# Optimization experiments

Measured on AMD Instinct MI355X. Metric: run time of the kernel, lower is better.

Reference implementation:

```python
import jax, jax.numpy as jnp
import numpy as np

B, L, D_MODEL, H = 2, 1920, 512, 8
DEPTH = D_MODEL // H
MAX_REL = 1921


def skew(t):
    """Huang et al. 2018 skew: pad, reshape, slice. t: (..., L, L)."""
    Lq, Lk = t.shape[-2], t.shape[-1]
    padded = jnp.pad(t, [(0, 0)] * (t.ndim - 1) + [(1, 0)])  # (..., Lq, Lk+1)
    s = padded.reshape(-1, Lk + 1, Lq)[:, 1:]                 # drop first row
    return s.reshape(t.shape)


def setup_inputs() -> dict:
    key = jax.random.key(0)
    ks = jax.random.split(key, 12)
    w = lambda k, shp: (jax.random.normal(k, shp, jnp.float32) * 0.02)
    inp = {
        "q": jax.random.normal(ks[0], (B, L, D_MODEL), jnp.float32),
        "k": jax.random.normal(ks[1], (B, L, D_MODEL), jnp.float32),
        "v": jax.random.normal(ks[2], (B, L, D_MODEL), jnp.float32),
        "mask": jnp.triu(jnp.ones((L, L), jnp.float32), k=1)[None, None],  # causal look-ahead
        "Wq": w(ks[3], (D_MODEL, D_MODEL)), "bq": jnp.zeros((D_MODEL,), jnp.float32),
        "Wk": w(ks[4], (D_MODEL, D_MODEL)), "bk": jnp.zeros((D_MODEL,), jnp.float32),
        "Wv": w(ks[5], (D_MODEL, D_MODEL)), "bv": jnp.zeros((D_MODEL,), jnp.float32),
        "E": w(ks[6], (MAX_REL, D_MODEL)),
        "Wo": w(ks[7], (D_MODEL, D_MODEL)), "bo": jnp.zeros((D_MODEL,), jnp.float32),
    }
    return inp


def reference(q, k, v, mask, Wq, bq, Wk, bk, Wv, bv, E, Wo, bo):
    Lk = k.shape[-2]
    qp = q @ Wq + bq
    kp = k @ Wk + bk
    vp = v @ Wv + bv
    # required relative embeddings (max_len >= seq_len branch): rightmost Lk rows
    e = E[MAX_REL - Lk:]                                   # (Lk, d_model)
    # split heads
    qh = qp.reshape(B, -1, H, DEPTH).transpose(0, 2, 1, 3)  # (B,H,Lq,depth)
    kh = kp.reshape(B, Lk, H, DEPTH).transpose(0, 2, 1, 3)
    vh = vp.reshape(B, Lk, H, DEPTH).transpose(0, 2, 1, 3)
    eh = e.reshape(Lk, H, DEPTH).transpose(1, 0, 2)         # (H,Lk,depth)
    QKt = jnp.einsum('bhqd,bhkd->bhqk', qh, kh)
    Srel = skew(jnp.einsum('bhqd,hkd->bhqk', qh, eh))
    logits = (QKt + Srel) / jnp.sqrt(jnp.float32(DEPTH))
    logits = logits + mask * (-1e9)
    attn = jax.nn.softmax(logits, axis=-1)                  # (B,H,Lq,Lk)
    out = jnp.einsum('bhqk,bhkd->bhqd', attn, vh)
    out = out.transpose(0, 2, 1, 3).reshape(B, -1, D_MODEL)
    out = out @ Wo + bo
    return out, attn
```

## Files before the change

kernel.cpp:

```cpp
#include <hip/hip_runtime.h>

typedef unsigned short u16;
typedef short s16x8 __attribute__((ext_vector_type(8)));
typedef float f32x4 __attribute__((ext_vector_type(4)));

#define MFMA_BF16(a, b, c) __builtin_amdgcn_mfma_f32_16x16x32_bf16((a), (b), (c), 0, 0, 0)

#define L_SEQ 1920
#define DM    512
#define NH    8
#define CH    6
#define NCHB  90

__device__ __forceinline__ u16 f2b(float f) {
  union { float f; unsigned u; } a; a.f = f;
  unsigned u = a.u;
  u += 0x7fffu + ((u >> 16) & 1u);
  return (u16)(u >> 16);
}
__device__ __forceinline__ float b2f(u16 h) {
  union { unsigned u; float f; } a; a.u = ((unsigned)h) << 16;
  return a.f;
}
__device__ __forceinline__ float rsum16(float x) {
  x += __shfl_xor(x, 1);
  x += __shfl_xor(x, 2);
  x += __shfl_xor(x, 4);
  x += __shfl_xor(x, 8);
  return x;
}

__global__ __launch_bounds__(256) void cvt_kernel(
    const float* __restrict__ q, const float* __restrict__ k,
    const float* __restrict__ v, const float* __restrict__ E,
    u16* __restrict__ qc, u16* __restrict__ kc,
    u16* __restrict__ vc, u16* __restrict__ Ec) {
  const float* src; u16* dst; int n;
  if (blockIdx.y == 0)      { src = q; dst = qc; n = 1966080; }
  else if (blockIdx.y == 1) { src = k; dst = kc; n = 1966080; }
  else if (blockIdx.y == 2) { src = v; dst = vc; n = 1966080; }
  else                      { src = E; dst = Ec; n = 983552; }
  const int i = (blockIdx.x * 256 + threadIdx.x) * 8;
  if (i < n) {
    float4 a = *(const float4*)(src + i);
    float4 b = *(const float4*)(src + i + 4);
    ushort4 ua; ua.x = f2b(a.x); ua.y = f2b(a.y); ua.z = f2b(a.z); ua.w = f2b(a.w);
    ushort4 ub; ub.x = f2b(b.x); ub.y = f2b(b.y); ub.z = f2b(b.z); ub.w = f2b(b.w);
    *(ushort4*)(dst + i)     = ua;
    *(ushort4*)(dst + i + 4) = ub;
  }
}

__global__ __launch_bounds__(256) void wtrans_kernel(
    const float* __restrict__ Wq, const float* __restrict__ Wk,
    const float* __restrict__ Wv, const float* __restrict__ Wo,
    u16* __restrict__ Wqt, u16* __restrict__ Wkt,
    u16* __restrict__ Wvt, u16* __restrict__ Wot) {
  const float* W; u16* Wt;
  if (blockIdx.z == 0)      { W = Wq; Wt = Wqt; }
  else if (blockIdx.z == 1) { W = Wk; Wt = Wkt; }
  else if (blockIdx.z == 2) { W = Wv; Wt = Wvt; }
  else                      { W = Wo; Wt = Wot; }
  const int k0 = blockIdx.y * 64, n0 = blockIdx.x * 64;
  __shared__ u16 T[64][72];
  const int r = threadIdx.x >> 2, c = (threadIdx.x & 3) * 16;
#pragma unroll
  for (int i = 0; i < 4; ++i) {
    float4 f = *(const float4*)(W + (size_t)(k0 + r) * 512 + n0 + c + i * 4);
    ushort4 u; u.x = f2b(f.x); u.y = f2b(f.y); u.z = f2b(f.z); u.w = f2b(f.w);
    *(ushort4*)&T[r][c + i * 4] = u;
  }
  __syncthreads();
  u16 tmp[16];
#pragma unroll
  for (int i = 0; i < 16; ++i) tmp[i] = T[c + i][r];
  u16* dst = Wt + (size_t)(n0 + r) * 512 + k0 + c;
  *(uint4*)dst       = *(uint4*)tmp;
  *(uint4*)(dst + 8) = *(uint4*)(tmp + 8);
}

__global__ __launch_bounds__(256) void vtrans_kernel(const u16* __restrict__ vp,
                                                     u16* __restrict__ vt) {
  const int bh = blockIdx.y, k0 = blockIdx.x * 64;
  const int b = bh >> 3, h = bh & 7;
  __shared__ u16 T[64][72];
  const int r = threadIdx.x >> 2, c = (threadIdx.x & 3) * 16;
  const u16* src = vp + (size_t)(b * L_SEQ + k0 + r) * DM + h * 64 + c;
  *(uint4*)&T[r][c]     = *(const uint4*)src;
  *(uint4*)&T[r][c + 8] = *(const uint4*)(src + 8);
  __syncthreads();
  u16 tmp[16];
#pragma unroll
  for (int i = 0; i < 16; ++i) tmp[i] = T[c + i][r];
  u16* dst = vt + (size_t)bh * 64 * L_SEQ + (size_t)r * L_SEQ + k0 + c;
  *(uint4*)dst       = *(uint4*)tmp;
  *(uint4*)(dst + 8) = *(uint4*)(tmp + 8);
}

template<bool OBF>
__device__ __forceinline__ void gemm512_body(const u16* Ap, const u16* Wt,
                                             const float* bias, void* Cp) {
  __shared__ u16 As[128][40];
  __shared__ u16 Bs[128][40];
  const int tid  = threadIdx.x;
  const int wv   = tid >> 6, lane = tid & 63, quad = lane >> 4, l16 = lane & 15;
  const int wr   = wv >> 1, wc = wv & 1;
  const int row0 = blockIdx.x * 128, n0 = blockIdx.y * 128;

  f32x4 acc[4][4];
#pragma unroll
  for (int i = 0; i < 4; ++i)
#pragma unroll
    for (int j = 0; j < 4; ++j) acc[i][j] = {0.f, 0.f, 0.f, 0.f};

  for (int kt = 0; kt < 16; ++kt) {
    const int k0 = kt * 32;
    const int r = tid >> 1, cs = (tid & 1) * 16;
    {
      const u16* src = Ap + (size_t)(row0 + r) * 512 + k0 + cs;
      *(uint4*)&As[r][cs]     = *(const uint4*)src;
      *(uint4*)&As[r][cs + 8] = *(const uint4*)(src + 8);
    }
    {
      const u16* src = Wt + (size_t)(n0 + r) * 512 + k0 + cs;
      *(uint4*)&Bs[r][cs]     = *(const uint4*)src;
      *(uint4*)&Bs[r][cs + 8] = *(const uint4*)(src + 8);
    }
    __syncthreads();
    s16x8 af[4], bfr[4];
#pragma unroll
    for (int i = 0; i < 4; ++i) af[i]  = *(const s16x8*)&As[wr * 64 + i * 16 + l16][quad * 8];
#pragma unroll
    for (int i = 0; i < 4; ++i) bfr[i] = *(const s16x8*)&Bs[wc * 64 + i * 16 + l16][quad * 8];
#pragma unroll
    for (int am = 0; am < 4; ++am)
#pragma unroll
      for (int bn = 0; bn < 4; ++bn)
        acc[am][bn] = MFMA_BF16(af[am], bfr[bn], acc[am][bn]);
    __syncthreads();
  }

#pragma unroll
  for (int am = 0; am < 4; ++am)
#pragma unroll
    for (int bn = 0; bn < 4; ++bn)
#pragma unroll
      for (int r = 0; r < 4; ++r) {
        const int row = row0 + wr * 64 + am * 16 + quad * 4 + r;
        const int col = n0 + wc * 64 + bn * 16 + l16;
        float v = acc[am][bn][r] + bias[col];
        if constexpr (OBF) ((u16*)Cp)[(size_t)row * 512 + col] = f2b(v);
        else               ((float*)Cp)[(size_t)row * 512 + col] = v;
      }
}

__global__ __launch_bounds__(256) void proj3_kernel(
    const u16* __restrict__ qc, const u16* __restrict__ kc, const u16* __restrict__ vc,
    const u16* __restrict__ Wqt, const u16* __restrict__ Wkt, const u16* __restrict__ Wvt,
    const float* __restrict__ bq, const float* __restrict__ bk, const float* __restrict__ bv,
    u16* __restrict__ qp, u16* __restrict__ kp, u16* __restrict__ vp) {
  const u16* A; const u16* W; const float* bias; u16* C;
  if (blockIdx.z == 0)      { A = qc; W = Wqt; bias = bq; C = qp; }
  else if (blockIdx.z == 1) { A = kc; W = Wkt; bias = bk; C = kp; }
  else                      { A = vc; W = Wvt; bias = bv; C = vp; }
  gemm512_body<true>(A, W, bias, C);
}

__global__ __launch_bounds__(256) void outproj_kernel(
    const u16* __restrict__ A, const u16* __restrict__ Wot,
    const float* __restrict__ bo, float* __restrict__ out) {
  gemm512_body<false>(A, Wot, bo, out);
}

__global__ __launch_bounds__(256) void flash_kernel(
    const u16* __restrict__ qp, const u16* __restrict__ kp, const u16* __restrict__ vt,
    const u16* __restrict__ Ec, u16* __restrict__ phat,
    float* __restrict__ opart, float* __restrict__ spart) {
  __shared__ u16 Qs[64][72];
  __shared__ u16 Ks[64][72];
  __shared__ u16 Vs[64][72];
  __shared__ u16 Es[128][72];
  __shared__ u16 PW[4][16][136];

  const int h = blockIdx.y, b = blockIdx.z;
  const int tid = threadIdx.x, wv = tid >> 6, lane = tid & 63;
  const int quad = lane >> 4, l16 = lane & 15;
  const int j0 = 48 - wv * 16;
  const int bh = b * NH + h;

  int qt = 0, c = blockIdx.x;
  for (;;) { const int n = (qt + CH) / CH; if (c < n) break; c -= n; ++qt; }
  const int kts = c * CH, kte = min(qt, kts + CH - 1);
  const int q0 = qt * 64;
  const size_t gcid = (size_t)bh * NCHB + blockIdx.x;

  const u16* qb = qp + (size_t)b * L_SEQ * DM + h * 64;
  const u16* kb = kp + (size_t)b * L_SEQ * DM + h * 64;
  const u16* vtb = vt + (size_t)bh * 64 * L_SEQ;
  const u16* Eb = Ec + h * 64;
  u16* pb = phat + ((size_t)bh * L_SEQ + q0) * L_SEQ;

  {
    const int r = tid >> 2, cc = (tid & 3) * 16;
    const u16* src = qb + (size_t)(q0 + r) * DM + cc;
    *(uint4*)&Qs[r][cc]     = *(const uint4*)src;
    *(uint4*)&Qs[r][cc + 8] = *(const uint4*)(src + 8);
  }

  float sr[4] = {0.f, 0.f, 0.f, 0.f};
  f32x4 oacc[4];
#pragma unroll
  for (int i = 0; i < 4; ++i) oacc[i] = {0.f, 0.f, 0.f, 0.f};

  for (int kt = kts; kt <= kte; ++kt) {
    const int k0 = kt * 64;
    {
      const int r = tid >> 2, cc = (tid & 3) * 16;
      const u16* src = kb + (size_t)(k0 + r) * DM + cc;
      *(uint4*)&Ks[r][cc]     = *(const uint4*)src;
      *(uint4*)&Ks[r][cc + 8] = *(const uint4*)(src + 8);
    }
    {
      const int d = tid >> 2, cc = (tid & 3) * 16;
      const u16* src = vtb + (size_t)d * L_SEQ + k0 + cc;
      *(uint4*)&Vs[d][cc]     = *(const uint4*)src;
      *(uint4*)&Vs[d][cc + 8] = *(const uint4*)(src + 8);
    }
    {
      const int j = tid >> 1, c2 = (tid & 1) * 32;
      int rg = k0 + (L_SEQ - 64) - q0 + j;
      rg = rg < 0 ? 0 : (rg > L_SEQ - 1 ? L_SEQ - 1 : rg);
      const u16* src = Eb + (size_t)(1 + rg) * DM + c2;
#pragma unroll
      for (int i = 0; i < 4; ++i)
        *(uint4*)&Es[j][c2 + i * 8] = *(const uint4*)(src + i * 8);
    }
    __syncthreads();

    f32x4 qa[4], ba[5];
#pragma unroll
    for (int i = 0; i < 4; ++i) qa[i] = {0.f, 0.f, 0.f, 0.f};
#pragma unroll
    for (int i = 0; i < 5; ++i) ba[i] = {0.f, 0.f, 0.f, 0.f};
#pragma unroll
    for (int kk = 0; kk < 2; ++kk) {
      s16x8 a = *(const s16x8*)&Qs[wv * 16 + l16][kk * 32 + quad * 8];
#pragma unroll
      for (int t = 0; t < 4; ++t) {
        s16x8 kf = *(const s16x8*)&Ks[t * 16 + l16][kk * 32 + quad * 8];
        qa[t] = MFMA_BF16(a, kf, qa[t]);
      }
#pragma unroll
      for (int u = 0; u < 5; ++u) {
        s16x8 ef = *(const s16x8*)&Es[j0 + u * 16 + l16][kk * 32 + quad * 8];
        ba[u] = MFMA_BF16(a, ef, ba[u]);
      }
    }
#pragma unroll
    for (int u = 0; u < 5; ++u)
#pragma unroll
      for (int r = 0; r < 4; ++r)
        PW[wv][quad * 4 + r][u * 16 + l16] = f2b(ba[u][r]);

    u16 pb16[4][4];
#pragma unroll
    for (int r = 0; r < 4; ++r) {
      const int lr = quad * 4 + r;
      const int qi = wv * 16 + lr;
      float ssum = 0.f;
#pragma unroll
      for (int t = 0; t < 4; ++t) {
        const float srel = b2f(PW[wv][lr][15 - lr + 16 * t + l16]);
        const float v = (qa[t][r] + srel) * 0.125f;
        const float p = ((k0 + t * 16 + l16) <= (q0 + qi)) ? __expf(v) : 0.f;
        ssum += p;
        const u16 pc = f2b(p);
        pb16[r][t] = pc;
        pb[(size_t)qi * L_SEQ + k0 + t * 16 + l16] = pc;
      }
      sr[r] += rsum16(ssum);
    }
#pragma unroll
    for (int t = 0; t < 4; ++t)
#pragma unroll
      for (int r = 0; r < 4; ++r)
        PW[wv][quad * 4 + r][t * 16 + l16] = pb16[r][t];

#pragma unroll
    for (int kk = 0; kk < 2; ++kk) {
      s16x8 pa = *(const s16x8*)&PW[wv][l16][kk * 32 + quad * 8];
#pragma unroll
      for (int db = 0; db < 4; ++db) {
        s16x8 vf = *(const s16x8*)&Vs[db * 16 + l16][kk * 32 + quad * 8];
        oacc[db] = MFMA_BF16(pa, vf, oacc[db]);
      }
    }
    __syncthreads();
  }

  float* op = opart + gcid * 4096;
#pragma unroll
  for (int db = 0; db < 4; ++db)
#pragma unroll
    for (int r = 0; r < 4; ++r)
      op[(size_t)(wv * 16 + quad * 4 + r) * 64 + db * 16 + l16] = oacc[db][r];
  if (l16 == 0) {
#pragma unroll
    for (int r = 0; r < 4; ++r)
      spart[gcid * 64 + wv * 16 + quad * 4 + r] = sr[r];
  }
}

__global__ __launch_bounds__(256) void merge_kernel(
    const float* __restrict__ opart, const float* __restrict__ spart,
    u16* __restrict__ oc, float* __restrict__ sfin) {
  const int qt = blockIdx.x, bh = blockIdx.y;
  const int b = bh >> 3, h = bh & 7;
  int pre = 0;
  for (int q2 = 0; q2 < qt; ++q2) pre += (q2 + CH) / CH;
  const int nc = (qt + CH) / CH;
  const size_t gc0 = (size_t)bh * NCHB + pre;

  const int qi = threadIdx.x >> 2, ds = (threadIdx.x & 3) * 16;
  float s = 0.f;
  float4 o[4] = {{0,0,0,0},{0,0,0,0},{0,0,0,0},{0,0,0,0}};
  for (int ci = 0; ci < nc; ++ci) {
    s += spart[(gc0 + ci) * 64 + qi];
    const float* op = opart + (gc0 + ci) * 4096 + (size_t)qi * 64 + ds;
#pragma unroll
    for (int i = 0; i < 4; ++i) {
      const float4 a = *(const float4*)(op + i * 4);
      o[i].x += a.x; o[i].y += a.y; o[i].z += a.z; o[i].w += a.w;
    }
  }
  const float inv = 1.0f / s;
  u16* dst = oc + (size_t)(b * L_SEQ + qt * 64 + qi) * DM + h * 64 + ds;
#pragma unroll
  for (int i = 0; i < 4; ++i) {
    ushort4 u;
    u.x = f2b(o[i].x * inv); u.y = f2b(o[i].y * inv);
    u.z = f2b(o[i].z * inv); u.w = f2b(o[i].w * inv);
    *(ushort4*)(dst + i * 4) = u;
  }
  if ((threadIdx.x & 3) == 0) sfin[(size_t)bh * L_SEQ + qt * 64 + qi] = s;
}

__global__ __launch_bounds__(256) void fixup_kernel(
    const u16* __restrict__ phat, const float* __restrict__ sfin,
    float* __restrict__ attn) {
  const int r = blockIdx.x, bh = blockIdx.y;
  const int nlow = ((r >> 6) + 1) * 64;
  const size_t rowidx = (size_t)bh * L_SEQ + r;
  const u16* prow = phat + rowidx * L_SEQ;
  float* arow = attn + rowidx * L_SEQ;
  const int g = threadIdx.x;
  if (g >= 240) return;
  const int col = g * 8;
  float4 o0, o1;
  if (col < nlow) {
    const float fac = 1.0f / sfin[rowidx];
    uint4 u = *(const uint4*)(prow + col);
    o0.x = b2f((u16)(u.x & 0xffff)) * fac;  o0.y = b2f((u16)(u.x >> 16)) * fac;
    o0.z = b2f((u16)(u.y & 0xffff)) * fac;  o0.w = b2f((u16)(u.y >> 16)) * fac;
    o1.x = b2f((u16)(u.z & 0xffff)) * fac;  o1.y = b2f((u16)(u.z >> 16)) * fac;
    o1.z = b2f((u16)(u.w & 0xffff)) * fac;  o1.w = b2f((u16)(u.w >> 16)) * fac;
  } else {
    o0 = {0.f, 0.f, 0.f, 0.f};
    o1 = {0.f, 0.f, 0.f, 0.f};
  }
  *(float4*)(arow + col)     = o0;
  *(float4*)(arow + col + 4) = o1;
}

extern "C" void kernel_launch(void* const* d_in, const int* in_sizes, int n_in,
                              void* d_out, int out_size, void* d_ws, size_t ws_size,
                              hipStream_t stream) {
  const float* q  = (const float*)d_in[0];
  const float* k  = (const float*)d_in[1];
  const float* v  = (const float*)d_in[2];
  const float* Wq = (const float*)d_in[4];
  const float* bq = (const float*)d_in[5];
  const float* Wk = (const float*)d_in[6];
  const float* bk = (const float*)d_in[7];
  const float* Wv = (const float*)d_in[8];
  const float* bv = (const float*)d_in[9];
  const float* E  = (const float*)d_in[10];
  const float* Wo = (const float*)d_in[11];
  const float* bo = (const float*)d_in[12];

  float* out  = (float*)d_out;
  float* attn = out + (size_t)3840 * 512;

  u16* qc  = (u16*)d_ws;
  u16* kc  = qc + 1966080;
  u16* vc  = kc + 1966080;
  u16* Wqt = vc + 1966080;
  u16* Wkt = Wqt + 262144;
  u16* Wvt = Wkt + 262144;
  u16* Wot = Wvt + 262144;
  u16* Ec  = Wot + 262144;
  u16* qp  = Ec + 983552;
  u16* kp  = qp + 1966080;
  u16* vp  = kp + 1966080;
  u16* vt  = vp + 1966080;
  u16* oc  = vt + 1966080;
  u16* phat = oc + 1966080;
  float* opart = (float*)(phat + 58982400);
  float* spart = opart + (size_t)1440 * 4096;
  float* sfin  = spart + 1440 * 64;

  cvt_kernel<<<dim3(960, 4), 256, 0, stream>>>(q, k, v, E, qc, kc, vc, Ec);
  wtrans_kernel<<<dim3(8, 8, 4), 256, 0, stream>>>(Wq, Wk, Wv, Wo, Wqt, Wkt, Wvt, Wot);
  proj3_kernel<<<dim3(30, 4, 3), 256, 0, stream>>>(qc, kc, vc, Wqt, Wkt, Wvt,
                                                   bq, bk, bv, qp, kp, vp);
  vtrans_kernel<<<dim3(30, 16), 256, 0, stream>>>(vp, vt);
  flash_kernel<<<dim3(NCHB, 8, 2), 256, 0, stream>>>(qp, kp, vt, Ec, phat, opart, spart);
  merge_kernel<<<dim3(30, 16), 256, 0, stream>>>(opart, spart, oc, sfin);
  fixup_kernel<<<dim3(1920, 16), 256, 0, stream>>>(phat, sfin, attn);
  outproj_kernel<<<dim3(30, 4), 256, 0, stream>>>(oc, Wot, bo, out);
}
```

Before: 429.3 us.

## Use direct global-to-LDS loads in GEMM, swizzle flash grid, vectorize P stores

```diff
diff --git a/kernel.cpp b/kernel.cpp
--- a/kernel.cpp
+++ b/kernel.cpp
@@ -11,6 +11,10 @@
 #define NH    8
 #define CH    6
 #define NCHB  90
+
+#define GLL16(gp, lp) __builtin_amdgcn_global_load_lds(                       \
+    (const __attribute__((address_space(1))) void*)(gp),                      \
+    (__attribute__((address_space(3))) void*)(lp), 16, 0, 0)
 
 __device__ __forceinline__ u16 f2b(float f) {
   union { float f; unsigned u; } a; a.f = f;
@@ -100,13 +104,17 @@
 template<bool OBF>
 __device__ __forceinline__ void gemm512_body(const u16* Ap, const u16* Wt,
                                              const float* bias, void* Cp) {
-  __shared__ u16 As[128][40];
-  __shared__ u16 Bs[128][40];
+  __shared__ u16 As[128 * 32];
+  __shared__ u16 Bs[128 * 32];
   const int tid  = threadIdx.x;
   const int wv   = tid >> 6, lane = tid & 63, quad = lane >> 4, l16 = lane & 15;
   const int wr   = wv >> 1, wc = wv & 1;
   const int row0 = blockIdx.x * 128, n0 = blockIdx.y * 128;
 
+  const int srow = tid >> 2, scol = (tid & 3) * 8;
+  const u16* sA = Ap + (size_t)(row0 + srow) * 512 + scol;
+  const u16* sB = Wt + (size_t)(n0  + srow) * 512 + scol;
+
   f32x4 acc[4][4];
 #pragma unroll
   for (int i = 0; i < 4; ++i)
@@ -115,23 +123,18 @@
 
   for (int kt = 0; kt < 16; ++kt) {
     const int k0 = kt * 32;
-    const int r = tid >> 1, cs = (tid & 1) * 16;
-    {
-      const u16* src = Ap + (size_t)(row0 + r) * 512 + k0 + cs;
-      *(uint4*)&As[r][cs]     = *(const uint4*)src;
-      *(uint4*)&As[r][cs + 8] = *(const uint4*)(src + 8);
-    }
-    {
-      const u16* src = Wt + (size_t)(n0 + r) * 512 + k0 + cs;
-      *(uint4*)&Bs[r][cs]     = *(const uint4*)src;
-      *(uint4*)&Bs[r][cs + 8] = *(const uint4*)(src + 8);
-    }
+    GLL16(sA + k0,             &As[wv * 512]);
+    GLL16(sA + k0 + 64 * 512,  &As[2048 + wv * 512]);
+    GLL16(sB + k0,             &Bs[wv * 512]);
+    GLL16(sB + k0 + 64 * 512,  &Bs[2048 + wv * 512]);
     __syncthreads();
     s16x8 af[4], bfr[4];
 #pragma unroll
-    for (int i = 0; i < 4; ++i) af[i]  = *(const s16x8*)&As[wr * 64 + i * 16 + l16][quad * 8];
-#pragma unroll
-    for (int i = 0; i < 4; ++i) bfr[i] = *(const s16x8*)&Bs[wc * 64 + i * 16 + l16][quad * 8];
+    for (int i = 0; i < 4; ++i)
+      af[i]  = *(const s16x8*)&As[(wr * 64 + i * 16 + l16) * 32 + quad * 8];
+#pragma unroll
+    for (int i = 0; i < 4; ++i)
+      bfr[i] = *(const s16x8*)&Bs[(wc * 64 + i * 16 + l16) * 32 + quad * 8];
 #pragma unroll
     for (int am = 0; am < 4; ++am)
 #pragma unroll
@@ -182,17 +185,21 @@
   __shared__ u16 Es[128][72];
   __shared__ u16 PW[4][16][136];
 
-  const int h = blockIdx.y, b = blockIdx.z;
+  const int wg  = blockIdx.x;
+  const int swz = (wg & 7) * 180 + (wg >> 3);
+  const int cid0 = swz % NCHB;
+  const int bh   = swz / NCHB;
+  const int h = bh & 7, b = bh >> 3;
+
   const int tid = threadIdx.x, wv = tid >> 6, lane = tid & 63;
   const int quad = lane >> 4, l16 = lane & 15;
   const int j0 = 48 - wv * 16;
-  const int bh = b * NH + h;
-
-  int qt = 0, c = blockIdx.x;
+
+  int qt = 0, c = cid0;
   for (;;) { const int n = (qt + CH) / CH; if (c < n) break; c -= n; ++qt; }
   const int kts = c * CH, kte = min(qt, kts + CH - 1);
   const int q0 = qt * 64;
-  const size_t gcid = (size_t)bh * NCHB + blockIdx.x;
+  const size_t gcid = (size_t)bh * NCHB + cid0;
 
   const u16* qb = qp + (size_t)b * L_SEQ * DM + h * 64;
   const u16* kb = kp + (size_t)b * L_SEQ * DM + h * 64;
@@ -274,9 +281,7 @@
         const float v = (qa[t][r] + srel) * 0.125f;
         const float p = ((k0 + t * 16 + l16) <= (q0 + qi)) ? __expf(v) : 0.f;
         ssum += p;
-        const u16 pc = f2b(p);
-        pb16[r][t] = pc;
-        pb[(size_t)qi * L_SEQ + k0 + t * 16 + l16] = pc;
+        pb16[r][t] = f2b(p);
       }
       sr[r] += rsum16(ssum);
     }
@@ -294,6 +299,14 @@
         s16x8 vf = *(const s16x8*)&Vs[db * 16 + l16][kk * 32 + quad * 8];
         oacc[db] = MFMA_BF16(pa, vf, oacc[db]);
       }
+    }
+
+    {
+      const int prow = lane >> 3, pcol = (lane & 7) * 8;
+      u16* d0 = pb + (size_t)(wv * 16 + prow) * L_SEQ + k0 + pcol;
+      u16* d1 = pb + (size_t)(wv * 16 + 8 + prow) * L_SEQ + k0 + pcol;
+      *(uint4*)d0 = *(const uint4*)&PW[wv][prow][pcol];
+      *(uint4*)d1 = *(const uint4*)&PW[wv][8 + prow][pcol];
     }
     __syncthreads();
   }
@@ -414,7 +427,7 @@
   proj3_kernel<<<dim3(30, 4, 3), 256, 0, stream>>>(qc, kc, vc, Wqt, Wkt, Wvt,
                                                    bq, bk, bv, qp, kp, vp);
   vtrans_kernel<<<dim3(30, 16), 256, 0, stream>>>(vp, vt);
-  flash_kernel<<<dim3(NCHB, 8, 2), 256, 0, stream>>>(qp, kp, vt, Ec, phat, opart, spart);
+  flash_kernel<<<dim3(1440), 256, 0, stream>>>(qp, kp, vt, Ec, phat, opart, spart);
   merge_kernel<<<dim3(30, 16), 256, 0, stream>>>(opart, spart, oc, sfin);
   fixup_kernel<<<dim3(1920, 16), 256, 0, stream>>>(phat, sfin, attn);
   outproj_kernel<<<dim3(30, 4), 256, 0, stream>>>(oc, Wot, bo, out);
```

Measured after the change: 414.8 us. -3.4%, faster.
